# Kernel tuning notes

Hardware: AMD Instinct MI355X
Metric: run time of the kernel (lower is better)

Reference implementation:

```python
import jax, jax.numpy as jnp
import numpy as np

B, S, DM = 2, 2048, 2048
H, KVH, HD = 16, 4, 128
REP = H // KVH  # kv_repeat_factor = 4
ROPE_BASE = 10000.0
EPS = 1e-6


def setup_inputs() -> dict:
    key = jax.random.key(0)
    k0, k1, k2, k3, k4 = jax.random.split(key, 5)
    w = lambda k, o, i: jax.random.normal(k, (o, i), jnp.float32) * (1.0 / np.sqrt(i))
    return {
        "x": jax.random.normal(k0, (B, S, DM), jnp.float32),
        "Wq": w(k1, H * HD, DM),
        "Wk": w(k2, KVH * HD, DM),
        "Wv": w(k3, KVH * HD, DM),
        "Wo": w(k4, DM, H * HD),
    }


def _rope_tables(seq_len, dim):
    inv_freq = 1.0 / (ROPE_BASE ** (jnp.arange(0, dim, 2, dtype=jnp.float32) / dim))
    t = jnp.arange(seq_len, dtype=jnp.float32)
    freqs = jnp.outer(t, inv_freq)            # [S, dim/2]
    emb = jnp.concatenate([freqs, freqs], -1)  # [S, dim]
    return jnp.cos(emb), jnp.sin(emb)


def _rotate_half(x):
    d = x.shape[-1] // 2
    return jnp.concatenate([-x[..., d:], x[..., :d]], axis=-1)


def reference(x, Wq, Wk, Wv, Wo):
    bsz, seq_len, _ = x.shape
    # projections (torch Linear: y = x @ W.T)
    q = (x @ Wq.T).reshape(bsz, seq_len, H, HD).transpose(0, 2, 1, 3)    # [B,H,S,D]
    k = (x @ Wk.T).reshape(bsz, seq_len, KVH, HD).transpose(0, 2, 1, 3)  # [B,KVH,S,D]
    v = (x @ Wv.T).reshape(bsz, seq_len, KVH, HD).transpose(0, 2, 1, 3)
    # rotary embeddings
    cos, sin = _rope_tables(seq_len, HD)  # [S,D]
    cos, sin = cos[None, None], sin[None, None]
    q = q * cos + _rotate_half(q) * sin
    k = k * cos + _rotate_half(k) * sin
    # GQA repeat (repeat_interleave on head dim)
    k = jnp.repeat(k, REP, axis=1)  # [B,H,S,D]
    v = jnp.repeat(v, REP, axis=1)
    # feature map
    qf = jax.nn.elu(q) + 1.0
    kf = jax.nn.elu(k) + 1.0
    # causal linear attention: recurrent kv-state scan over time
    qf_t = qf.transpose(2, 0, 1, 3)  # [S,B,H,D]
    kf_t = kf.transpose(2, 0, 1, 3)
    v_t = v.transpose(2, 0, 1, 3)

    def step(carry, inp):
        state, z = carry                       # [B,H,D,D], [B,H,D]
        q_s, k_s, v_s = inp                    # each [B,H,D]
        state = state + k_s[..., :, None] * v_s[..., None, :]
        z = z + k_s
        num = jnp.einsum('bhe,bhed->bhd', q_s, state)
        den = jnp.einsum('bhe,bhe->bh', q_s, z)[..., None] + EPS
        return (state, z), num / den

    init = (jnp.zeros((bsz, H, HD, HD), x.dtype), jnp.zeros((bsz, H, HD), x.dtype))
    _, out = jax.lax.scan(step, init, (qf_t, kf_t, v_t))  # [S,B,H,D]
    out = out.transpose(1, 0, 2, 3).reshape(bsz, seq_len, H * HD)
    return out @ Wo.T
```

## Files before the change

### kernel.cpp

```cpp
#include <hip/hip_runtime.h>
#include <math.h>
#include <stdint.h>

#define B_ 2
#define S_ 2048
#define H_ 16
#define KVH_ 4
#define HD_ 128
#define NC_ 16
#define CHK_ 128
#define EPS_ 1e-6f
#define GK_ 2048
#define NT_ (GK_ / 32)

typedef __attribute__((ext_vector_type(8))) short short8;
typedef __attribute__((ext_vector_type(4))) float f32x4;

#define GLOAD16(gsrc, sdst) \
    __builtin_amdgcn_global_load_lds((const __attribute__((address_space(1))) unsigned int*)(gsrc), \
                                     (__attribute__((address_space(3))) unsigned int*)(sdst), 16, 0, 0)

static __device__ __forceinline__ float bf2f(unsigned int u) {
    return __uint_as_float(u << 16);
}

static __device__ __forceinline__ void pack8(const float* v, uint4& hi, uint4& lo) {
    unsigned int h[4], l[4];
#pragma unroll
    for (int w = 0; w < 4; w++) {
        unsigned int b0 = __float_as_uint(v[2 * w]);
        unsigned int b1 = __float_as_uint(v[2 * w + 1]);
        unsigned int h0 = b0 & 0xFFFF0000u, h1 = b1 & 0xFFFF0000u;
        h[w] = (h0 >> 16) | h1;
        float r0 = v[2 * w] - __uint_as_float(h0);
        float r1 = v[2 * w + 1] - __uint_as_float(h1);
        l[w] = (__float_as_uint(r0) >> 16) | (__float_as_uint(r1) & 0xFFFF0000u);
    }
    hi = make_uint4(h[0], h[1], h[2], h[3]);
    lo = make_uint4(l[0], l[1], l[2], l[3]);
}

static __device__ __forceinline__ void split8_frag(const float* p, short8& hi, short8& lo) {
#pragma unroll
    for (int e = 0; e < 8; e++) {
        unsigned int b = __float_as_uint(p[e]);
        unsigned int h = b & 0xFFFF0000u;
        hi[e] = (short)(h >> 16);
        float r = p[e] - __uint_as_float(h);
        lo[e] = (short)(__float_as_uint(r) >> 16);
    }
}

__global__ __launch_bounds__(256) void rope_tables_k(float* __restrict__ cost,
                                                     float* __restrict__ sint) {
    int idx = blockIdx.x * 256 + threadIdx.x;
    int j = idx & 63;
    int s = idx >> 6;
    float inv_freq = powf(10000.0f, -(float)(2 * j) / 128.0f);
    float f = (float)s * inv_freq;
    cost[idx] = cosf(f);
    sint[idx] = sinf(f);
}

__global__ __launch_bounds__(256) void split_in_k(
    const float* __restrict__ x,  const float* __restrict__ wq,
    const float* __restrict__ wk, const float* __restrict__ wv,
    unsigned int* __restrict__ xpk,  unsigned int* __restrict__ wqpk,
    unsigned int* __restrict__ wkpk, unsigned int* __restrict__ wvpk)
{
    int g = blockIdx.x * 256 + threadIdx.x;
    const float* in;
    unsigned int* outp;
    int lg;
    if (g < 1048576)      { in = x;  outp = xpk;  lg = g; }
    else if (g < 1572864) { in = wq; outp = wqpk; lg = g - 1048576; }
    else if (g < 1703936) { in = wk; outp = wkpk; lg = g - 1572864; }
    else                  { in = wv; outp = wvpk; lg = g - 1703936; }
    const float* p = in + (size_t)lg * 8;
    float v[8];
    *(float4*)&v[0] = *(const float4*)p;
    *(float4*)&v[4] = *(const float4*)(p + 4);
    uint4 hi, lo;
    pack8(v, hi, lo);
    unsigned int* op = outp + (size_t)lg * 8;
    *(uint4*)op       = hi;
    *(uint4*)(op + 4) = lo;
}

__global__ __launch_bounds__(256) void split_k(const float* __restrict__ in,
                                               unsigned int* __restrict__ outp, int ngrp)
{
    int g = blockIdx.x * 256 + threadIdx.x;
    if (g >= ngrp) return;
    const float* p = in + (size_t)g * 8;
    float x[8];
    *(float4*)&x[0] = *(const float4*)p;
    *(float4*)&x[4] = *(const float4*)(p + 4);
    uint4 hi, lo;
    pack8(x, hi, lo);
    unsigned int* op = outp + (size_t)g * 8;
    *(uint4*)op       = hi;
    *(uint4*)(op + 4) = lo;
}

template <int EPI>
__global__ __launch_bounds__(256, 2) void gemm3_k(
    const char* __restrict__ Apk, const char* __restrict__ W0,
    const char* __restrict__ W1, const char* __restrict__ W2,
    float* __restrict__ Y, int ldY, int nend0, int nend1, int nbx,
    const float* __restrict__ cosT, const float* __restrict__ sinT,
    char* __restrict__ qfo, char* __restrict__ kfo, float* __restrict__ vvo)
{
    __shared__ __attribute__((aligned(16))) char smem[65536];

    int nwg = gridDim.x;
    int bid = blockIdx.x;
    int swz = (bid & 7) * (nwg >> 3) + (bid >> 3);
    int by = swz / nbx, bx = swz % nbx;
    const int m0 = by * 128, n0 = bx * 128;

    const char* Wsel;
    int nw;
    if (n0 < nend0)      { Wsel = W0; nw = n0; }
    else if (n0 < nend1) { Wsel = W1; nw = n0 - nend0; }
    else                 { Wsel = W2; nw = n0 - nend1; }

    const int tid = threadIdx.x;
    const int lane = tid & 63;
    const int wv = tid >> 6;
    const int wr = wv >> 1, wc = wv & 1;

    const int r8 = lane >> 3, sl = lane & 7;
    const char* ap[4];
    const char* wp[4];
    int adst[4], wdst[4];
#pragma unroll
    for (int i = 0; i < 4; i++) {
        int rowA = wv * 32 + i * 8 + r8;
        ap[i] = Apk + (size_t)(m0 + rowA) * (GK_ * 4) + (size_t)((sl ^ (rowA & 7)) * 16);
        wp[i] = Wsel + (size_t)(nw + rowA) * (GK_ * 4) + (size_t)((sl ^ (rowA & 7)) * 16);
        adst[i] = wv * 4096 + i * 1024;
        wdst[i] = 16384 + wv * 4096 + i * 1024;
    }

    const int lrow = lane & 15, lg = lane >> 4, lc7 = lane & 7;
    const int aoff = (wr * 64 + lrow) * 128 + ((((lg << 1)) ^ lc7) << 4);
    const int woff = 16384 + (wc * 64 + lrow) * 128 + ((((lg << 1)) ^ lc7) << 4);

    f32x4 acc[4][4];
#pragma unroll
    for (int i = 0; i < 4; i++)
#pragma unroll
        for (int j = 0; j < 4; j++) acc[i][j] = (f32x4)(0.f);

#pragma unroll
    for (int i = 0; i < 4; i++) {
        GLOAD16(ap[i], smem + adst[i]);
        GLOAD16(wp[i], smem + wdst[i]);
    }
    __syncthreads();

    for (int kt = 0; kt < NT_; ++kt) {
        const int cur = kt & 1;
        if (kt + 1 < NT_) {
            const size_t koff = (size_t)(kt + 1) * 128;
            const int nb = (cur ^ 1) * 32768;
#pragma unroll
            for (int i = 0; i < 4; i++) {
                GLOAD16(ap[i] + koff, smem + nb + adst[i]);
                GLOAD16(wp[i] + koff, smem + nb + wdst[i]);
            }
        }
        const char* sb = smem + cur * 32768;
        short8 ah[4], al[4], bh[4], bl[4];
#pragma unroll
        for (int f = 0; f < 4; f++) {
            ah[f] = *(const short8*)(sb + (aoff)        + f * 2048);
            al[f] = *(const short8*)(sb + (aoff ^ 16)   + f * 2048);
            bh[f] = *(const short8*)(sb + (woff)        + f * 2048);
            bl[f] = *(const short8*)(sb + (woff ^ 16)   + f * 2048);
        }
#pragma unroll
        for (int i = 0; i < 4; i++)
#pragma unroll
            for (int j = 0; j < 4; j++) {
                acc[i][j] = __builtin_amdgcn_mfma_f32_16x16x32_bf16(ah[i], bh[j], acc[i][j], 0, 0, 0);
                acc[i][j] = __builtin_amdgcn_mfma_f32_16x16x32_bf16(ah[i], bl[j], acc[i][j], 0, 0, 0);
                acc[i][j] = __builtin_amdgcn_mfma_f32_16x16x32_bf16(al[i], bh[j], acc[i][j], 0, 0, 0);
            }
        __syncthreads();
    }

    if (EPI == 0) {
#pragma unroll
        for (int i = 0; i < 4; i++) {
            int r0 = m0 + wr * 64 + i * 16 + lg * 4;
#pragma unroll
            for (int j = 0; j < 4; j++) {
                int cc = n0 + wc * 64 + j * 16 + lrow;
                f32x4 v = acc[i][j];
                Y[(size_t)(r0 + 0) * ldY + cc] = v[0];
                Y[(size_t)(r0 + 1) * ldY + cc] = v[1];
                Y[(size_t)(r0 + 2) * ldY + cc] = v[2];
                Y[(size_t)(r0 + 3) * ldY + cc] = v[3];
            }
        }
    } else {
        float* Ct = (float*)smem;
#pragma unroll
        for (int i = 0; i < 4; i++) {
            int r = wr * 64 + i * 16 + lg * 4;
#pragma unroll
            for (int j = 0; j < 4; j++) {
                int ccol = wc * 64 + j * 16 + lrow;
#pragma unroll
                for (int rr = 0; rr < 4; rr++)
                    Ct[(r + rr) * 128 + ccol] = acc[i][j][rr];
            }
        }
        __syncthreads();
        if (n0 < 2560) {
            const int isq = (n0 < 2048) ? 1 : 0;
            const int hh = isq ? (n0 >> 7) : ((n0 - 2048) >> 7);
            char* basep = isq ? qfo : kfo;
            const int bstride = (isq ? H_ : KVH_) * S_;
#pragma unroll
            for (int it = 0; it < 8; it++) {
                int idx = it * 256 + tid;
                int row = idx >> 4, g = idx & 15;
                int midx = m0 + row, bb = midx >> 11, ss = midx & 2047;
                int j0 = g * 8;
                int lowh = (j0 < 64) ? 1 : 0;
                int f0 = lowh ? j0 : j0 - 64;
                float o[8];
#pragma unroll
                for (int e = 0; e < 8; e++) {
                    float cs = cosT[ss * 64 + f0 + e];
                    float sn = sinT[ss * 64 + f0 + e];
                    float a = Ct[row * 128 + j0 + e];
                    float p = Ct[row * 128 + (lowh ? j0 + e + 64 : j0 + e - 64)];
                    float v = lowh ? (a * cs - p * sn) : (a * cs + p * sn);
                    o[e] = v > 0.f ? v + 1.f : expf(v);
                }
                uint4 hi, lo;
                pack8(o, hi, lo);
                char* dst = basep + ((size_t)bb * bstride + (size_t)hh * S_ + ss) * 512 + g * 32;
                *(uint4*)dst        = hi;
                *(uint4*)(dst + 16) = lo;
            }
        } else {
            const int kvh = (n0 - 2560) >> 7;
#pragma unroll
            for (int it = 0; it < 16; it++) {
                int idx = it * 256 + tid;
                int r = idx >> 5, c4 = idx & 31;
                int midx = m0 + r, bb = midx >> 11, ss = midx & 2047;
                *(float4*)(vvo + ((size_t)(bb * KVH_ + kvh) * S_ + ss) * HD_ + c4 * 4) =
                    *(const float4*)(Ct + r * 128 + c4 * 4);
            }
        }
    }
}

__global__ __launch_bounds__(256) void vt_k(const float* __restrict__ vv,
                                            char* __restrict__ vtpk)
{
    __shared__ __attribute__((aligned(16))) float Vt[CHK_][HD_ + 4];
    int bx = blockIdx.x;
    int st = bx & 15;
    int bkv = bx >> 4;
    int tid = threadIdx.x;
#pragma unroll
    for (int it = 0; it < 16; it++) {
        int idx = it * 256 + tid;
        int r = idx >> 5, c4 = idx & 31;
        *(float4*)&Vt[r][c4 * 4] =
            *(const float4*)(vv + ((size_t)bkv * S_ + st * CHK_ + r) * HD_ + c4 * 4);
    }
    __syncthreads();
#pragma unroll
    for (int it = 0; it < 2; it++) {
        int t2 = it * 256 + tid;
        int d = t2 & 127, sg = t2 >> 7;
#pragma unroll
        for (int kk = 0; kk < 4; kk++) {
            int kgl = sg * 4 + kk;
            float f[8];
#pragma unroll
            for (int e = 0; e < 8; e++) f[e] = Vt[kgl * 8 + e][d];
            uint4 hi, lo;
            pack8(f, hi, lo);
            char* op = vtpk + (size_t)bkv * 1048576 + (size_t)d * 8192 + (size_t)(st * 16 + kgl) * 32;
            *(uint4*)op        = hi;
            *(uint4*)(op + 16) = lo;
        }
    }
}

__global__ __launch_bounds__(256) void chunk_kv_k(
    const char* __restrict__ kfpk, const float* __restrict__ vv,
    float* __restrict__ kvc, float* __restrict__ zc)
{
    int bx = blockIdx.x;
    int c = bx % NC_;
    int bkv = bx / NC_;
    const char* kp = kfpk + ((size_t)bkv * S_ + c * CHK_) * 512;
    const float* vp = vv + ((size_t)bkv * S_ + c * CHK_) * HD_;
    __shared__ __attribute__((aligned(16))) float ks[CHK_][HD_ + 4];
    __shared__ __attribute__((aligned(16))) float vs[CHK_][HD_ + 4];
    int tid = threadIdx.x, tx = tid & 15, ty = tid >> 4;
#pragma unroll
    for (int it = 0; it < 8; it++) {
        int idx = it * 256 + tid;
        int r = idx >> 4, kg = idx & 15;
        const uint4* sp = (const uint4*)(kp + (size_t)r * 512 + kg * 32);
        uint4 hi = sp[0], lo = sp[1];
        float* d = &ks[r][kg * 8];
        d[0] = bf2f(hi.x & 0xFFFFu) + bf2f(lo.x & 0xFFFFu);
        d[1] = bf2f(hi.x >> 16)     + bf2f(lo.x >> 16);
        d[2] = bf2f(hi.y & 0xFFFFu) + bf2f(lo.y & 0xFFFFu);
        d[3] = bf2f(hi.y >> 16)     + bf2f(lo.y >> 16);
        d[4] = bf2f(hi.z & 0xFFFFu) + bf2f(lo.z & 0xFFFFu);
        d[5] = bf2f(hi.z >> 16)     + bf2f(lo.z >> 16);
        d[6] = bf2f(hi.w & 0xFFFFu) + bf2f(lo.w & 0xFFFFu);
        d[7] = bf2f(hi.w >> 16)     + bf2f(lo.w >> 16);
    }
#pragma unroll
    for (int it = 0; it < 16; it++) {
        int idx = it * 256 + tid;
        int r = idx >> 5, c4 = idx & 31;
        *(float4*)&vs[r][c4 * 4] = *(const float4*)(vp + (size_t)r * HD_ + c4 * 4);
    }
    __syncthreads();
    float acc[8][8];
#pragma unroll
    for (int i = 0; i < 8; i++)
#pragma unroll
        for (int j = 0; j < 8; j++) acc[i][j] = 0.f;
    for (int j = 0; j < CHK_; j++) {
        float a[8], b[8];
        *(float4*)&a[0] = *(const float4*)&ks[j][ty * 8];
        *(float4*)&a[4] = *(const float4*)&ks[j][ty * 8 + 4];
        *(float4*)&b[0] = *(const float4*)&vs[j][tx * 8];
        *(float4*)&b[4] = *(const float4*)&vs[j][tx * 8 + 4];
#pragma unroll
        for (int i = 0; i < 8; i++)
#pragma unroll
            for (int jj = 0; jj < 8; jj++)
                acc[i][jj] = fmaf(a[i], b[jj], acc[i][jj]);
    }
    float* outp = kvc + (size_t)bx * (HD_ * HD_);
#pragma unroll
    for (int i = 0; i < 8; i++) {
        float* op = outp + (size_t)(ty * 8 + i) * HD_ + tx * 8;
        *(float4*)op       = make_float4(acc[i][0], acc[i][1], acc[i][2], acc[i][3]);
        *(float4*)(op + 4) = make_float4(acc[i][4], acc[i][5], acc[i][6], acc[i][7]);
    }
    if (tid < CHK_) {
        float z = 0.f;
        for (int j = 0; j < CHK_; j++) z += ks[j][tid];
        zc[(size_t)bx * HD_ + tid] = z;
    }
}

__global__ __launch_bounds__(256) void chunk_scan_k(const float* __restrict__ kvc,
                                                    char* __restrict__ kvct,
                                                    float* __restrict__ zc)
{
    int bx = blockIdx.x;
    int bkv = bx >> 3, dg = bx & 7;
    int tid = threadIdx.x;
    int d = dg * 16 + (tid & 15);
    int g8 = tid >> 4;
    float acc[8];
#pragma unroll
    for (int i = 0; i < 8; i++) acc[i] = 0.f;
    float zacc = 0.f;
    for (int c = 0; c < NC_; c++) {
        size_t cb = (size_t)(bkv * NC_ + c);
        const float* p = kvc + cb * 16384;
        float cur[8];
#pragma unroll
        for (int i = 0; i < 8; i++) cur[i] = p[(g8 * 8 + i) * 128 + d];
        uint4 hi, lo;
        pack8(acc, hi, lo);
        char* op = kvct + cb * 65536 + (size_t)d * 512 + g8 * 32;
        *(uint4*)op        = hi;
        *(uint4*)(op + 16) = lo;
#pragma unroll
        for (int i = 0; i < 8; i++) acc[i] += cur[i];
        if (tid < 16) {
            float* zp = zc + cb * 128 + dg * 16 + tid;
            float zcur = *zp;
            *zp = zacc;
            zacc += zcur;
        }
    }
}

__global__ __launch_bounds__(256, 1) void chunk_out_k(
    const char* __restrict__ qfpk, const char* __restrict__ kfpk,
    const char* __restrict__ vtpk, const char* __restrict__ kvct,
    const float* __restrict__ zc, char* __restrict__ attnpk)
{
    __shared__ __attribute__((aligned(16))) char smem[100864];
    char*  stA  = smem;
    char*  stB  = smem + 16384;
    float* Pf   = (float*)(smem + 32768);
    float* zs   = (float*)(smem + 98304);
    float* rsum = (float*)(smem + 98816);
    float* den2 = (float*)(smem + 99840);
    float* den  = (float*)(smem + 100352);

    int bx = blockIdx.x;
    int c = bx & 15, h = (bx >> 4) & 15, b = bx >> 8;
    int kv = h >> 2;
    int bkv = b * KVH_ + kv;
    int bkvc = bkv * NC_ + c;
    const char* Qb  = qfpk + ((size_t)(b * H_ + h) * S_ + c * CHK_) * 512;
    const char* Kb  = kfpk + ((size_t)bkv * S_ + c * CHK_) * 512;
    const char* Vtb = vtpk + (size_t)bkv * 1048576 + (size_t)c * 512;
    const char* Spb = kvct + (size_t)bkvc * 65536;
    const float* zp = zc + (size_t)bkvc * 128;

    int tid = threadIdx.x;
    int lane = tid & 63, wv = tid >> 6;
    int wr = wv >> 1, wc = wv & 1;
    int lrow = lane & 15, lg = lane >> 4, l7 = lane & 7;

    if (tid < 32) *(float4*)(zs + tid * 4) = *(const float4*)(zp + tid * 4);

    const char *qsrc[4], *ksrc[4], *vsrc[4], *ssrc[4];
    char *adst[4], *bdst[4];
#pragma unroll
    for (int i = 0; i < 4; i++) {
        int row = wv * 32 + i * 8 + (lane >> 3);
        int sl = (lane & 7) ^ (row & 7);
        qsrc[i] = Qb  + (size_t)row * 512  + sl * 16;
        ksrc[i] = Kb  + (size_t)row * 512  + sl * 16;
        vsrc[i] = Vtb + (size_t)row * 8192 + sl * 16;
        ssrc[i] = Spb + (size_t)row * 512  + sl * 16;
        adst[i] = stA + wv * 4096 + i * 1024;
        bdst[i] = stB + wv * 4096 + i * 1024;
    }
    int aoffs[4], boffs[4];
#pragma unroll
    for (int f = 0; f < 4; f++) {
        aoffs[f] = (wr * 64 + f * 16 + lrow) * 128 + (((lg << 1) ^ l7) << 4);
        boffs[f] = (wc * 64 + f * 16 + lrow) * 128 + (((lg << 1) ^ l7) << 4);
    }

    f32x4 acc1[4][4];
#pragma unroll
    for (int i = 0; i < 4; i++)
#pragma unroll
        for (int j = 0; j < 4; j++) acc1[i][j] = (f32x4)(0.f);

    for (int s = 0; s < 4; s++) {
#pragma unroll
        for (int i = 0; i < 4; i++) {
            GLOAD16(qsrc[i] + s * 128, adst[i]);
            GLOAD16(ksrc[i] + s * 128, bdst[i]);
        }
        __syncthreads();
        short8 ah[4], al[4], bh[4], bl[4];
#pragma unroll
        for (int f = 0; f < 4; f++) {
            ah[f] = *(const short8*)(stA + aoffs[f]);
            al[f] = *(const short8*)(stA + (aoffs[f] ^ 16));
            bh[f] = *(const short8*)(stB + boffs[f]);
            bl[f] = *(const short8*)(stB + (boffs[f] ^ 16));
        }
#pragma unroll
        for (int i = 0; i < 4; i++)
#pragma unroll
            for (int j = 0; j < 4; j++) {
                acc1[i][j] = __builtin_amdgcn_mfma_f32_16x16x32_bf16(ah[i], bh[j], acc1[i][j], 0, 0, 0);
                acc1[i][j] = __builtin_amdgcn_mfma_f32_16x16x32_bf16(ah[i], bl[j], acc1[i][j], 0, 0, 0);
                acc1[i][j] = __builtin_amdgcn_mfma_f32_16x16x32_bf16(al[i], bh[j], acc1[i][j], 0, 0, 0);
            }
        __syncthreads();
    }

#pragma unroll
    for (int fi = 0; fi < 4; fi++) {
#pragma unroll
        for (int reg = 0; reg < 4; reg++) {
            int i = wr * 64 + fi * 16 + lg * 4 + reg;
            float rsv = 0.f;
#pragma unroll
            for (int fj = 0; fj < 4; fj++) {
                int j = wc * 64 + fj * 16 + lrow;
                float v = (j <= i) ? acc1[fi][fj][reg] : 0.f;
                rsv += v;
                Pf[i * 128 + (((j >> 3) ^ (i & 7)) << 3) + (j & 7)] = v;
            }
#pragma unroll
            for (int m = 1; m < 16; m <<= 1) rsv += __shfl_xor(rsv, m, 64);
            if (lrow == 0) rsum[i * 2 + wc] = rsv;
        }
    }

    f32x4 acc2[4][4];
#pragma unroll
    for (int i = 0; i < 4; i++)
#pragma unroll
        for (int j = 0; j < 4; j++) acc2[i][j] = (f32x4)(0.f);
    float d2a[4] = {0.f, 0.f, 0.f, 0.f};

    for (int s = 0; s < 4; s++) {
#pragma unroll
        for (int i = 0; i < 4; i++) {
            GLOAD16(qsrc[i] + s * 128, adst[i]);
            GLOAD16(ssrc[i] + s * 128, bdst[i]);
        }
        __syncthreads();
        short8 ah[4], al[4], bh[4], bl[4];
#pragma unroll
        for (int f = 0; f < 4; f++) {
            ah[f] = *(const short8*)(stA + aoffs[f]);
            al[f] = *(const short8*)(stA + (aoffs[f] ^ 16));
            bh[f] = *(const short8*)(stB + boffs[f]);
            bl[f] = *(const short8*)(stB + (boffs[f] ^ 16));
        }
        float zv[8];
#pragma unroll
        for (int e = 0; e < 8; e++) zv[e] = zs[s * 32 + lg * 8 + e];
#pragma unroll
        for (int f = 0; f < 4; f++)
#pragma unroll
            for (int e = 0; e < 8; e++)
                d2a[f] += (bf2f((unsigned int)(unsigned short)ah[f][e]) +
                           bf2f((unsigned int)(unsigned short)al[f][e])) * zv[e];
#pragma unroll
        for (int i = 0; i < 4; i++)
#pragma unroll
            for (int j = 0; j < 4; j++) {
                acc2[i][j] = __builtin_amdgcn_mfma_f32_16x16x32_bf16(ah[i], bh[j], acc2[i][j], 0, 0, 0);
                acc2[i][j] = __builtin_amdgcn_mfma_f32_16x16x32_bf16(ah[i], bl[j], acc2[i][j], 0, 0, 0);
                acc2[i][j] = __builtin_amdgcn_mfma_f32_16x16x32_bf16(al[i], bh[j], acc2[i][j], 0, 0, 0);
            }
        __syncthreads();
    }
#pragma unroll
    for (int f = 0; f < 4; f++) {
        float v = d2a[f];
        v += __shfl_xor(v, 16, 64);
        v += __shfl_xor(v, 32, 64);
        if (wc == 0 && lg == 0) den2[wr * 64 + f * 16 + lrow] = v;
    }

    for (int s = 0; s < 4; s++) {
#pragma unroll
        for (int i = 0; i < 4; i++) GLOAD16(vsrc[i] + s * 128, bdst[i]);
        __syncthreads();
        short8 ph[4], pl[4], bh[4], bl[4];
#pragma unroll
        for (int f = 0; f < 4; f++) {
            int i = wr * 64 + f * 16 + lrow;
            int g = (s * 4 + lg) ^ (i & 7);
            float pv[8];
            *(float4*)&pv[0] = *(const float4*)(Pf + i * 128 + g * 8);
            *(float4*)&pv[4] = *(const float4*)(Pf + i * 128 + g * 8 + 4);
            split8_frag(pv, ph[f], pl[f]);
            bh[f] = *(const short8*)(stB + boffs[f]);
            bl[f] = *(const short8*)(stB + (boffs[f] ^ 16));
        }
#pragma unroll
        for (int i = 0; i < 4; i++)
#pragma unroll
            for (int j = 0; j < 4; j++) {
                acc2[i][j] = __builtin_amdgcn_mfma_f32_16x16x32_bf16(ph[i], bh[j], acc2[i][j], 0, 0, 0);
                acc2[i][j] = __builtin_amdgcn_mfma_f32_16x16x32_bf16(ph[i], bl[j], acc2[i][j], 0, 0, 0);
                acc2[i][j] = __builtin_amdgcn_mfma_f32_16x16x32_bf16(pl[i], bh[j], acc2[i][j], 0, 0, 0);
            }
        __syncthreads();
    }

    if (tid < 128) den[tid] = rsum[tid * 2] + rsum[tid * 2 + 1] + den2[tid] + EPS_;
    __syncthreads();
#pragma unroll
    for (int fi = 0; fi < 4; fi++) {
#pragma unroll
        for (int reg = 0; reg < 4; reg++) {
            int i = wr * 64 + fi * 16 + lg * 4 + reg;
            float inv = 1.0f / den[i];
#pragma unroll
            for (int fd = 0; fd < 4; fd++) {
                int d = wc * 64 + fd * 16 + lrow;
                Pf[i * 128 + (((d >> 3) ^ (i & 7)) << 3) + (d & 7)] = acc2[fi][fd][reg] * inv;
            }
        }
    }
    __syncthreads();
    int s0 = c * CHK_;
#pragma unroll
    for (int it = 0; it < 8; it++) {
        int idx = it * 256 + tid;
        int row = idx >> 4, kg = idx & 15;
        int g = kg ^ (row & 7);
        float f[8];
        *(float4*)&f[0] = *(const float4*)(Pf + row * 128 + g * 8);
        *(float4*)&f[4] = *(const float4*)(Pf + row * 128 + g * 8 + 4);
        uint4 hi, lo;
        pack8(f, hi, lo);
        char* op = attnpk + ((size_t)(b * S_ + s0 + row) * 256 + h * 16 + kg) * 32;
        *(uint4*)op        = hi;
        *(uint4*)(op + 16) = lo;
    }
}

extern "C" void kernel_launch(void* const* d_in, const int* in_sizes, int n_in,
                              void* d_out, int out_size, void* d_ws, size_t ws_size,
                              hipStream_t stream)
{
    (void)in_sizes; (void)n_in; (void)out_size; (void)ws_size;
    const float* x  = (const float*)d_in[0];
    const float* Wq = (const float*)d_in[1];
    const float* Wk = (const float*)d_in[2];
    const float* Wv = (const float*)d_in[3];
    const float* Wo = (const float*)d_in[4];
    float* out = (float*)d_out;
    float* ws  = (float*)d_ws;

    float* xpk   = ws;
    float* wqpk  = ws + 8388608;
    float* wkpk  = ws + 12582912;
    float* wvpk  = ws + 13631488;
    char*  qfpk  = (char*)(ws + 14680064);
    char*  kfpk  = (char*)(ws + 23068672);
    float* vv    = ws + 25165824;
    float* cost  = ws + 27262976;
    float* sint  = ws + 27394048;
    float* zc    = ws + 27525120;
    char*  vtpk   = (char*)(ws + 8388608);
    float* kvc    = ws + 10485760;
    char*  kvct   = (char*)(ws + 12582912);
    char*  attnpk = (char*)ws;
    float* wopk   = ws + 8388608;

    rope_tables_k<<<512, 256, 0, stream>>>(cost, sint);

    split_in_k<<<7168, 256, 0, stream>>>(x, Wq, Wk, Wv,
                                         (unsigned int*)xpk, (unsigned int*)wqpk,
                                         (unsigned int*)wkpk, (unsigned int*)wvpk);
    gemm3_k<1><<<768, 256, 0, stream>>>((const char*)xpk, (const char*)wqpk,
                                        (const char*)wkpk, (const char*)wvpk,
                                        nullptr, 0, 2048, 2560, 24,
                                        cost, sint, qfpk, kfpk, vv);

    vt_k<<<128, 256, 0, stream>>>(vv, vtpk);

    chunk_kv_k<<<B_ * KVH_ * NC_, 256, 0, stream>>>(kfpk, vv, kvc, zc);
    chunk_scan_k<<<64, 256, 0, stream>>>(kvc, kvct, zc);
    chunk_out_k<<<B_ * H_ * NC_, 256, 0, stream>>>(qfpk, kfpk, vtpk, kvct, zc, attnpk);

    split_k<<<2048, 256, 0, stream>>>(Wo, (unsigned int*)wopk, 524288);
    gemm3_k<0><<<512, 256, 0, stream>>>((const char*)attnpk, (const char*)wopk,
                                        (const char*)wopk, (const char*)wopk,
                                        out, 2048, 1 << 30, 1 << 30, 16,
                                        nullptr, nullptr, nullptr, nullptr, nullptr);
}
```

Before: 426.6 us.

## Rework projection GEMMs to 8-wave 256x128 tiles with triple-buffered LDS pipeline

The split-bf16 GEMM kernel now runs 512 threads (8 waves) per block on a 256x128 output tile, with a 3-stage LDS ring buffer (144 KB) that prefetches two K-steps ahead. Global-to-LDS loads are interleaved between the two MFMA halves, waits use explicit vmcnt counts, and MFMA sections are wrapped in setprio. The aim is to hide global load latency and halve redundant weight traffic per output. In exchange, each CU holds only one block, fewer blocks are launched, and the epilogue's shared-memory reuse and explicit waitcnt bookkeeping are more fragile.

```diff
diff --git a/kernel.cpp b/kernel.cpp
--- a/kernel.cpp
+++ b/kernel.cpp
@@ -11,7 +11,7 @@
 #define CHK_ 128
 #define EPS_ 1e-6f
 #define GK_ 2048
-#define NT_ (GK_ / 32)
+#define NT8_ (GK_ / 32)
 
 typedef __attribute__((ext_vector_type(8))) short short8;
 typedef __attribute__((ext_vector_type(4))) float f32x4;
@@ -19,6 +19,8 @@
 #define GLOAD16(gsrc, sdst) \
     __builtin_amdgcn_global_load_lds((const __attribute__((address_space(1))) unsigned int*)(gsrc), \
                                      (__attribute__((address_space(3))) unsigned int*)(sdst), 16, 0, 0)
+
+#define MFMA_B16(a, b, c) __builtin_amdgcn_mfma_f32_16x16x32_bf16((a), (b), (c), 0, 0, 0)
 
 static __device__ __forceinline__ float bf2f(unsigned int u) {
     return __uint_as_float(u << 16);
@@ -104,20 +106,20 @@
 }
 
 template <int EPI>
-__global__ __launch_bounds__(256, 2) void gemm3_k(
+__global__ __launch_bounds__(512, 1) void gemm8_k(
     const char* __restrict__ Apk, const char* __restrict__ W0,
     const char* __restrict__ W1, const char* __restrict__ W2,
     float* __restrict__ Y, int ldY, int nend0, int nend1, int nbx,
     const float* __restrict__ cosT, const float* __restrict__ sinT,
     char* __restrict__ qfo, char* __restrict__ kfo, float* __restrict__ vvo)
 {
-    __shared__ __attribute__((aligned(16))) char smem[65536];
+    __shared__ __attribute__((aligned(16))) char smem[147456];
 
     int nwg = gridDim.x;
     int bid = blockIdx.x;
     int swz = (bid & 7) * (nwg >> 3) + (bid >> 3);
     int by = swz / nbx, bx = swz % nbx;
-    const int m0 = by * 128, n0 = bx * 128;
+    const int m0 = by * 256, n0 = bx * 128;
 
     const char* Wsel;
     int nw;
@@ -128,24 +130,32 @@
     const int tid = threadIdx.x;
     const int lane = tid & 63;
     const int wv = tid >> 6;
-    const int wr = wv >> 1, wc = wv & 1;
+    const int wm = wv >> 1, wn = wv & 1;
 
     const int r8 = lane >> 3, sl = lane & 7;
-    const char* ap[4];
-    const char* wp[4];
-    int adst[4], wdst[4];
+    const char* asrc[4];
+    const char* bsrc[2];
+    int adst[4], bdst[2];
 #pragma unroll
     for (int i = 0; i < 4; i++) {
         int rowA = wv * 32 + i * 8 + r8;
-        ap[i] = Apk + (size_t)(m0 + rowA) * (GK_ * 4) + (size_t)((sl ^ (rowA & 7)) * 16);
-        wp[i] = Wsel + (size_t)(nw + rowA) * (GK_ * 4) + (size_t)((sl ^ (rowA & 7)) * 16);
+        asrc[i] = Apk + (size_t)(m0 + rowA) * (GK_ * 4) + (size_t)((sl ^ (rowA & 7)) * 16);
         adst[i] = wv * 4096 + i * 1024;
-        wdst[i] = 16384 + wv * 4096 + i * 1024;
+    }
+#pragma unroll
+    for (int j = 0; j < 2; j++) {
+        int rowB = wv * 16 + j * 8 + r8;
+        bsrc[j] = Wsel + (size_t)(nw + rowB) * (GK_ * 4) + (size_t)((sl ^ (rowB & 7)) * 16);
+        bdst[j] = 32768 + wv * 2048 + j * 1024;
     }
 
     const int lrow = lane & 15, lg = lane >> 4, lc7 = lane & 7;
-    const int aoff = (wr * 64 + lrow) * 128 + ((((lg << 1)) ^ lc7) << 4);
-    const int woff = 16384 + (wc * 64 + lrow) * 128 + ((((lg << 1)) ^ lc7) << 4);
+    int aoff[4], boff[4];
+#pragma unroll
+    for (int f = 0; f < 4; f++) {
+        aoff[f] = (wm * 64 + f * 16 + lrow) * 128 + (((lg << 1) ^ lc7) << 4);
+        boff[f] = 32768 + (wn * 64 + f * 16 + lrow) * 128 + (((lg << 1) ^ lc7) << 4);
+    }
 
     f32x4 acc[4][4];
 #pragma unroll
@@ -154,50 +164,88 @@
         for (int j = 0; j < 4; j++) acc[i][j] = (f32x4)(0.f);
 
 #pragma unroll
-    for (int i = 0; i < 4; i++) {
-        GLOAD16(ap[i], smem + adst[i]);
-        GLOAD16(wp[i], smem + wdst[i]);
-    }
-    __syncthreads();
-
-    for (int kt = 0; kt < NT_; ++kt) {
-        const int cur = kt & 1;
-        if (kt + 1 < NT_) {
-            const size_t koff = (size_t)(kt + 1) * 128;
-            const int nb = (cur ^ 1) * 32768;
-#pragma unroll
-            for (int i = 0; i < 4; i++) {
-                GLOAD16(ap[i] + koff, smem + nb + adst[i]);
-                GLOAD16(wp[i] + koff, smem + nb + wdst[i]);
-            }
-        }
-        const char* sb = smem + cur * 32768;
-        short8 ah[4], al[4], bh[4], bl[4];
+    for (int i = 0; i < 4; i++) GLOAD16(asrc[i], smem + adst[i]);
+#pragma unroll
+    for (int j = 0; j < 2; j++) GLOAD16(bsrc[j], smem + bdst[j]);
+#pragma unroll
+    for (int i = 0; i < 4; i++) GLOAD16(asrc[i] + 128, smem + 49152 + adst[i]);
+#pragma unroll
+    for (int j = 0; j < 2; j++) GLOAD16(bsrc[j] + 128, smem + 49152 + bdst[j]);
+    asm volatile("s_waitcnt vmcnt(6)" ::: "memory");
+    __builtin_amdgcn_s_barrier();
+    __builtin_amdgcn_sched_barrier(0);
+
+#pragma unroll 1
+    for (int kt = 0; kt < NT8_; ++kt) {
+        const char* sb = smem + (kt % 3) * 49152;
+        char* stp = smem + ((kt + 2) % 3) * 49152;
+        const size_t koff = (size_t)(kt + 2) * 128;
+        const bool st = (kt + 2 < NT8_);
+
+        if (st) {
+            GLOAD16(asrc[0] + koff, stp + adst[0]);
+            GLOAD16(asrc[1] + koff, stp + adst[1]);
+            GLOAD16(asrc[2] + koff, stp + adst[2]);
+        }
+        short8 bh[4], bl[4];
 #pragma unroll
         for (int f = 0; f < 4; f++) {
-            ah[f] = *(const short8*)(sb + (aoff)        + f * 2048);
-            al[f] = *(const short8*)(sb + (aoff ^ 16)   + f * 2048);
-            bh[f] = *(const short8*)(sb + (woff)        + f * 2048);
-            bl[f] = *(const short8*)(sb + (woff ^ 16)   + f * 2048);
-        }
-#pragma unroll
-        for (int i = 0; i < 4; i++)
+            bh[f] = *(const short8*)(sb + boff[f]);
+            bl[f] = *(const short8*)(sb + (boff[f] ^ 16));
+        }
+        short8 a0h = *(const short8*)(sb + aoff[0]);
+        short8 a0l = *(const short8*)(sb + (aoff[0] ^ 16));
+        short8 a1h = *(const short8*)(sb + aoff[1]);
+        short8 a1l = *(const short8*)(sb + (aoff[1] ^ 16));
+        __builtin_amdgcn_s_setprio(1);
+#pragma unroll
+        for (int j = 0; j < 4; j++) {
+            acc[0][j] = MFMA_B16(a0h, bh[j], acc[0][j]);
+            acc[0][j] = MFMA_B16(a0h, bl[j], acc[0][j]);
+            acc[0][j] = MFMA_B16(a0l, bh[j], acc[0][j]);
+            acc[1][j] = MFMA_B16(a1h, bh[j], acc[1][j]);
+            acc[1][j] = MFMA_B16(a1h, bl[j], acc[1][j]);
+            acc[1][j] = MFMA_B16(a1l, bh[j], acc[1][j]);
+        }
+        __builtin_amdgcn_s_setprio(0);
+        __builtin_amdgcn_s_barrier();
+
+        if (st) {
+            GLOAD16(asrc[3] + koff, stp + adst[3]);
+            GLOAD16(bsrc[0] + koff, stp + bdst[0]);
+            GLOAD16(bsrc[1] + koff, stp + bdst[1]);
+        }
+        short8 a2h = *(const short8*)(sb + aoff[2]);
+        short8 a2l = *(const short8*)(sb + (aoff[2] ^ 16));
+        short8 a3h = *(const short8*)(sb + aoff[3]);
+        short8 a3l = *(const short8*)(sb + (aoff[3] ^ 16));
+        __builtin_amdgcn_s_setprio(1);
+#pragma unroll
+        for (int j = 0; j < 4; j++) {
+            acc[2][j] = MFMA_B16(a2h, bh[j], acc[2][j]);
+            acc[2][j] = MFMA_B16(a2h, bl[j], acc[2][j]);
+            acc[2][j] = MFMA_B16(a2l, bh[j], acc[2][j]);
+            acc[3][j] = MFMA_B16(a3h, bh[j], acc[3][j]);
+            acc[3][j] = MFMA_B16(a3h, bl[j], acc[3][j]);
+            acc[3][j] = MFMA_B16(a3l, bh[j], acc[3][j]);
+        }
+        __builtin_amdgcn_s_setprio(0);
+        if (kt < NT8_ - 2) {
+            asm volatile("s_waitcnt vmcnt(6)" ::: "memory");
+        } else if (kt == NT8_ - 2) {
+            asm volatile("s_waitcnt vmcnt(0)" ::: "memory");
+        }
+        __builtin_amdgcn_s_barrier();
+        __builtin_amdgcn_sched_barrier(0);
+    }
+
+    if (EPI == 0) {
+#pragma unroll
+        for (int i = 0; i < 4; i++) {
+            int r0 = m0 + wm * 64 + i * 16 + lg * 4;
 #pragma unroll
             for (int j = 0; j < 4; j++) {
-                acc[i][j] = __builtin_amdgcn_mfma_f32_16x16x32_bf16(ah[i], bh[j], acc[i][j], 0, 0, 0);
-                acc[i][j] = __builtin_amdgcn_mfma_f32_16x16x32_bf16(ah[i], bl[j], acc[i][j], 0, 0, 0);
-                acc[i][j] = __builtin_amdgcn_mfma_f32_16x16x32_bf16(al[i], bh[j], acc[i][j], 0, 0, 0);
-            }
-        __syncthreads();
-    }
-
-    if (EPI == 0) {
-#pragma unroll
-        for (int i = 0; i < 4; i++) {
-            int r0 = m0 + wr * 64 + i * 16 + lg * 4;
-#pragma unroll
-            for (int j = 0; j < 4; j++) {
-                int cc = n0 + wc * 64 + j * 16 + lrow;
+                int cc = n0 + wn * 64 + j * 16 + lrow;
                 f32x4 v = acc[i][j];
                 Y[(size_t)(r0 + 0) * ldY + cc] = v[0];
                 Y[(size_t)(r0 + 1) * ldY + cc] = v[1];
@@ -209,10 +257,10 @@
         float* Ct = (float*)smem;
 #pragma unroll
         for (int i = 0; i < 4; i++) {
-            int r = wr * 64 + i * 16 + lg * 4;
+            int r = wm * 64 + i * 16 + lg * 4;
 #pragma unroll
             for (int j = 0; j < 4; j++) {
-                int ccol = wc * 64 + j * 16 + lrow;
+                int ccol = wn * 64 + j * 16 + lrow;
 #pragma unroll
                 for (int rr = 0; rr < 4; rr++)
                     Ct[(r + rr) * 128 + ccol] = acc[i][j][rr];
@@ -226,7 +274,7 @@
             const int bstride = (isq ? H_ : KVH_) * S_;
 #pragma unroll
             for (int it = 0; it < 8; it++) {
-                int idx = it * 256 + tid;
+                int idx = it * 512 + tid;
                 int row = idx >> 4, g = idx & 15;
                 int midx = m0 + row, bb = midx >> 11, ss = midx & 2047;
                 int j0 = g * 8;
@@ -252,7 +300,7 @@
             const int kvh = (n0 - 2560) >> 7;
 #pragma unroll
             for (int it = 0; it < 16; it++) {
-                int idx = it * 256 + tid;
+                int idx = it * 512 + tid;
                 int r = idx >> 5, c4 = idx & 31;
                 int midx = m0 + r, bb = midx >> 11, ss = midx & 2047;
                 *(float4*)(vvo + ((size_t)(bb * KVH_ + kvh) * S_ + ss) * HD_ + c4 * 4) =
@@ -475,9 +523,9 @@
         for (int i = 0; i < 4; i++)
 #pragma unroll
             for (int j = 0; j < 4; j++) {
-                acc1[i][j] = __builtin_amdgcn_mfma_f32_16x16x32_bf16(ah[i], bh[j], acc1[i][j], 0, 0, 0);
-                acc1[i][j] = __builtin_amdgcn_mfma_f32_16x16x32_bf16(ah[i], bl[j], acc1[i][j], 0, 0, 0);
-                acc1[i][j] = __builtin_amdgcn_mfma_f32_16x16x32_bf16(al[i], bh[j], acc1[i][j], 0, 0, 0);
+                acc1[i][j] = MFMA_B16(ah[i], bh[j], acc1[i][j]);
+                acc1[i][j] = MFMA_B16(ah[i], bl[j], acc1[i][j]);
+                acc1[i][j] = MFMA_B16(al[i], bh[j], acc1[i][j]);
             }
         __syncthreads();
     }
@@ -536,9 +584,9 @@
         for (int i = 0; i < 4; i++)
 #pragma unroll
             for (int j = 0; j < 4; j++) {
-                acc2[i][j] = __builtin_amdgcn_mfma_f32_16x16x32_bf16(ah[i], bh[j], acc2[i][j], 0, 0, 0);
-                acc2[i][j] = __builtin_amdgcn_mfma_f32_16x16x32_bf16(ah[i], bl[j], acc2[i][j], 0, 0, 0);
-                acc2[i][j] = __builtin_amdgcn_mfma_f32_16x16x32_bf16(al[i], bh[j], acc2[i][j], 0, 0, 0);
+                acc2[i][j] = MFMA_B16(ah[i], bh[j], acc2[i][j]);
+                acc2[i][j] = MFMA_B16(ah[i], bl[j], acc2[i][j]);
+                acc2[i][j] = MFMA_B16(al[i], bh[j], acc2[i][j]);
             }
         __syncthreads();
     }
@@ -570,9 +618,9 @@
         for (int i = 0; i < 4; i++)
 #pragma unroll
             for (int j = 0; j < 4; j++) {
-                acc2[i][j] = __builtin_amdgcn_mfma_f32_16x16x32_bf16(ph[i], bh[j], acc2[i][j], 0, 0, 0);
-                acc2[i][j] = __builtin_amdgcn_mfma_f32_16x16x32_bf16(ph[i], bl[j], acc2[i][j], 0, 0, 0);
-                acc2[i][j] = __builtin_amdgcn_mfma_f32_16x16x32_bf16(pl[i], bh[j], acc2[i][j], 0, 0, 0);
+                acc2[i][j] = MFMA_B16(ph[i], bh[j], acc2[i][j]);
+                acc2[i][j] = MFMA_B16(ph[i], bl[j], acc2[i][j]);
+                acc2[i][j] = MFMA_B16(pl[i], bh[j], acc2[i][j]);
             }
         __syncthreads();
     }
@@ -644,7 +692,7 @@
     split_in_k<<<7168, 256, 0, stream>>>(x, Wq, Wk, Wv,
                                          (unsigned int*)xpk, (unsigned int*)wqpk,
                                          (unsigned int*)wkpk, (unsigned int*)wvpk);
-    gemm3_k<1><<<768, 256, 0, stream>>>((const char*)xpk, (const char*)wqpk,
+    gemm8_k<1><<<384, 512, 0, stream>>>((const char*)xpk, (const char*)wqpk,
                                         (const char*)wkpk, (const char*)wvpk,
                                         nullptr, 0, 2048, 2560, 24,
                                         cost, sint, qfpk, kfpk, vv);
@@ -656,7 +704,7 @@
     chunk_out_k<<<B_ * H_ * NC_, 256, 0, stream>>>(qfpk, kfpk, vtpk, kvct, zc, attnpk);
 
     split_k<<<2048, 256, 0, stream>>>(Wo, (unsigned int*)wopk, 524288);
-    gemm3_k<0><<<512, 256, 0, stream>>>((const char*)attnpk, (const char*)wopk,
+    gemm8_k<0><<<256, 512, 0, stream>>>((const char*)attnpk, (const char*)wopk,
                                         (const char*)wopk, (const char*)wopk,
                                         out, 2048, 1 << 30, 1 << 30, 16,
                                         nullptr, nullptr, nullptr, nullptr, nullptr);
```

New measurement: 468.9 us. 1.1x slower.

## Fuse rope tables into split kernel and V transpose into chunk KV kernel

Applied to the files above, without the earlier changes.

Folds the rope cos/sin table generation into the input split kernel as extra blocks, and merges the V-transpose/pack kernel into the per-chunk KV state kernel. The chunk KV kernel is also split along the key dimension into two halves, which doubles the block count from 128 to 256 and halves per-thread accumulators. This removes two kernel launches and a separate reload of V, and improves occupancy of a small-grid kernel. The trade-off is that the half-1 blocks carry extra transpose work, which creates some load imbalance, and each block still loads the full V chunk.

```diff
diff --git a/kernel.cpp b/kernel.cpp
--- a/kernel.cpp
+++ b/kernel.cpp
@@ -20,6 +20,8 @@
     __builtin_amdgcn_global_load_lds((const __attribute__((address_space(1))) unsigned int*)(gsrc), \
                                      (__attribute__((address_space(3))) unsigned int*)(sdst), 16, 0, 0)
 
+#define MFMA_B16(a, b, c) __builtin_amdgcn_mfma_f32_16x16x32_bf16((a), (b), (c), 0, 0, 0)
+
 static __device__ __forceinline__ float bf2f(unsigned int u) {
     return __uint_as_float(u << 16);
 }
@@ -51,24 +53,24 @@
     }
 }
 
-__global__ __launch_bounds__(256) void rope_tables_k(float* __restrict__ cost,
-                                                     float* __restrict__ sint) {
-    int idx = blockIdx.x * 256 + threadIdx.x;
-    int j = idx & 63;
-    int s = idx >> 6;
-    float inv_freq = powf(10000.0f, -(float)(2 * j) / 128.0f);
-    float f = (float)s * inv_freq;
-    cost[idx] = cosf(f);
-    sint[idx] = sinf(f);
-}
-
 __global__ __launch_bounds__(256) void split_in_k(
     const float* __restrict__ x,  const float* __restrict__ wq,
     const float* __restrict__ wk, const float* __restrict__ wv,
     unsigned int* __restrict__ xpk,  unsigned int* __restrict__ wqpk,
-    unsigned int* __restrict__ wkpk, unsigned int* __restrict__ wvpk)
+    unsigned int* __restrict__ wkpk, unsigned int* __restrict__ wvpk,
+    float* __restrict__ cost, float* __restrict__ sint)
 {
     int g = blockIdx.x * 256 + threadIdx.x;
+    if (g >= 1835008) {
+        int idx = g - 1835008;
+        int j = idx & 63;
+        int s = idx >> 6;
+        float inv_freq = powf(10000.0f, -(float)(2 * j) / 128.0f);
+        float f = (float)s * inv_freq;
+        cost[idx] = cosf(f);
+        sint[idx] = sinf(f);
+        return;
+    }
     const float* in;
     unsigned int* outp;
     int lg;
@@ -184,9 +186,9 @@
         for (int i = 0; i < 4; i++)
 #pragma unroll
             for (int j = 0; j < 4; j++) {
-                acc[i][j] = __builtin_amdgcn_mfma_f32_16x16x32_bf16(ah[i], bh[j], acc[i][j], 0, 0, 0);
-                acc[i][j] = __builtin_amdgcn_mfma_f32_16x16x32_bf16(ah[i], bl[j], acc[i][j], 0, 0, 0);
-                acc[i][j] = __builtin_amdgcn_mfma_f32_16x16x32_bf16(al[i], bh[j], acc[i][j], 0, 0, 0);
+                acc[i][j] = MFMA_B16(ah[i], bh[j], acc[i][j]);
+                acc[i][j] = MFMA_B16(ah[i], bl[j], acc[i][j]);
+                acc[i][j] = MFMA_B16(al[i], bh[j], acc[i][j]);
             }
         __syncthreads();
     }
@@ -262,60 +264,26 @@
     }
 }
 
-__global__ __launch_bounds__(256) void vt_k(const float* __restrict__ vv,
-                                            char* __restrict__ vtpk)
-{
-    __shared__ __attribute__((aligned(16))) float Vt[CHK_][HD_ + 4];
-    int bx = blockIdx.x;
-    int st = bx & 15;
-    int bkv = bx >> 4;
-    int tid = threadIdx.x;
-#pragma unroll
-    for (int it = 0; it < 16; it++) {
-        int idx = it * 256 + tid;
-        int r = idx >> 5, c4 = idx & 31;
-        *(float4*)&Vt[r][c4 * 4] =
-            *(const float4*)(vv + ((size_t)bkv * S_ + st * CHK_ + r) * HD_ + c4 * 4);
-    }
-    __syncthreads();
-#pragma unroll
-    for (int it = 0; it < 2; it++) {
-        int t2 = it * 256 + tid;
-        int d = t2 & 127, sg = t2 >> 7;
-#pragma unroll
-        for (int kk = 0; kk < 4; kk++) {
-            int kgl = sg * 4 + kk;
-            float f[8];
-#pragma unroll
-            for (int e = 0; e < 8; e++) f[e] = Vt[kgl * 8 + e][d];
-            uint4 hi, lo;
-            pack8(f, hi, lo);
-            char* op = vtpk + (size_t)bkv * 1048576 + (size_t)d * 8192 + (size_t)(st * 16 + kgl) * 32;
-            *(uint4*)op        = hi;
-            *(uint4*)(op + 16) = lo;
-        }
-    }
-}
-
-__global__ __launch_bounds__(256) void chunk_kv_k(
+__global__ __launch_bounds__(256) void chunk_kvt_k(
     const char* __restrict__ kfpk, const float* __restrict__ vv,
-    float* __restrict__ kvc, float* __restrict__ zc)
+    float* __restrict__ kvc, float* __restrict__ zc, char* __restrict__ vtpk)
 {
     int bx = blockIdx.x;
-    int c = bx % NC_;
-    int bkv = bx / NC_;
+    int eh = bx & 1;
+    int c = (bx >> 1) & 15;
+    int bkv = bx >> 5;
     const char* kp = kfpk + ((size_t)bkv * S_ + c * CHK_) * 512;
     const float* vp = vv + ((size_t)bkv * S_ + c * CHK_) * HD_;
-    __shared__ __attribute__((aligned(16))) float ks[CHK_][HD_ + 4];
+    __shared__ __attribute__((aligned(16))) float ks[CHK_][68];
     __shared__ __attribute__((aligned(16))) float vs[CHK_][HD_ + 4];
     int tid = threadIdx.x, tx = tid & 15, ty = tid >> 4;
 #pragma unroll
-    for (int it = 0; it < 8; it++) {
+    for (int it = 0; it < 4; it++) {
         int idx = it * 256 + tid;
-        int r = idx >> 4, kg = idx & 15;
-        const uint4* sp = (const uint4*)(kp + (size_t)r * 512 + kg * 32);
+        int r = idx >> 3, kg8 = idx & 7;
+        const uint4* sp = (const uint4*)(kp + (size_t)r * 512 + (eh * 8 + kg8) * 32);
         uint4 hi = sp[0], lo = sp[1];
-        float* d = &ks[r][kg * 8];
+        float* d = &ks[r][kg8 * 8];
         d[0] = bf2f(hi.x & 0xFFFFu) + bf2f(lo.x & 0xFFFFu);
         d[1] = bf2f(hi.x >> 16)     + bf2f(lo.x >> 16);
         d[2] = bf2f(hi.y & 0xFFFFu) + bf2f(lo.y & 0xFFFFu);
@@ -332,34 +300,52 @@
         *(float4*)&vs[r][c4 * 4] = *(const float4*)(vp + (size_t)r * HD_ + c4 * 4);
     }
     __syncthreads();
-    float acc[8][8];
-#pragma unroll
-    for (int i = 0; i < 8; i++)
+    float acc[4][8];
+#pragma unroll
+    for (int i = 0; i < 4; i++)
 #pragma unroll
         for (int j = 0; j < 8; j++) acc[i][j] = 0.f;
     for (int j = 0; j < CHK_; j++) {
-        float a[8], b[8];
-        *(float4*)&a[0] = *(const float4*)&ks[j][ty * 8];
-        *(float4*)&a[4] = *(const float4*)&ks[j][ty * 8 + 4];
+        float a[4], b[8];
+        *(float4*)&a[0] = *(const float4*)&ks[j][ty * 4];
         *(float4*)&b[0] = *(const float4*)&vs[j][tx * 8];
         *(float4*)&b[4] = *(const float4*)&vs[j][tx * 8 + 4];
 #pragma unroll
-        for (int i = 0; i < 8; i++)
+        for (int i = 0; i < 4; i++)
 #pragma unroll
             for (int jj = 0; jj < 8; jj++)
                 acc[i][jj] = fmaf(a[i], b[jj], acc[i][jj]);
     }
-    float* outp = kvc + (size_t)bx * (HD_ * HD_);
-#pragma unroll
-    for (int i = 0; i < 8; i++) {
-        float* op = outp + (size_t)(ty * 8 + i) * HD_ + tx * 8;
+    float* outp = kvc + (size_t)(bkv * NC_ + c) * (HD_ * HD_);
+#pragma unroll
+    for (int i = 0; i < 4; i++) {
+        float* op = outp + (size_t)(eh * 64 + ty * 4 + i) * HD_ + tx * 8;
         *(float4*)op       = make_float4(acc[i][0], acc[i][1], acc[i][2], acc[i][3]);
         *(float4*)(op + 4) = make_float4(acc[i][4], acc[i][5], acc[i][6], acc[i][7]);
     }
-    if (tid < CHK_) {
+    if (tid < 64) {
         float z = 0.f;
         for (int j = 0; j < CHK_; j++) z += ks[j][tid];
-        zc[(size_t)bx * HD_ + tid] = z;
+        zc[(size_t)(bkv * NC_ + c) * HD_ + eh * 64 + tid] = z;
+    }
+    if (eh == 1) {
+#pragma unroll
+        for (int it = 0; it < 2; it++) {
+            int t2 = it * 256 + tid;
+            int d = t2 & 127, sg = t2 >> 7;
+#pragma unroll
+            for (int kk = 0; kk < 4; kk++) {
+                int kgl = sg * 4 + kk;
+                float f[8];
+#pragma unroll
+                for (int e = 0; e < 8; e++) f[e] = vs[kgl * 8 + e][d];
+                uint4 hi, lo;
+                pack8(f, hi, lo);
+                char* op = vtpk + (size_t)bkv * 1048576 + (size_t)d * 8192 + (size_t)(c * 16 + kgl) * 32;
+                *(uint4*)op        = hi;
+                *(uint4*)(op + 16) = lo;
+            }
+        }
     }
 }
 
@@ -475,9 +461,9 @@
         for (int i = 0; i < 4; i++)
 #pragma unroll
             for (int j = 0; j < 4; j++) {
-                acc1[i][j] = __builtin_amdgcn_mfma_f32_16x16x32_bf16(ah[i], bh[j], acc1[i][j], 0, 0, 0);
-                acc1[i][j] = __builtin_amdgcn_mfma_f32_16x16x32_bf16(ah[i], bl[j], acc1[i][j], 0, 0, 0);
-                acc1[i][j] = __builtin_amdgcn_mfma_f32_16x16x32_bf16(al[i], bh[j], acc1[i][j], 0, 0, 0);
+                acc1[i][j] = MFMA_B16(ah[i], bh[j], acc1[i][j]);
+                acc1[i][j] = MFMA_B16(ah[i], bl[j], acc1[i][j]);
+                acc1[i][j] = MFMA_B16(al[i], bh[j], acc1[i][j]);
             }
         __syncthreads();
     }
@@ -536,9 +522,9 @@
         for (int i = 0; i < 4; i++)
 #pragma unroll
             for (int j = 0; j < 4; j++) {
-                acc2[i][j] = __builtin_amdgcn_mfma_f32_16x16x32_bf16(ah[i], bh[j], acc2[i][j], 0, 0, 0);
-                acc2[i][j] = __builtin_amdgcn_mfma_f32_16x16x32_bf16(ah[i], bl[j], acc2[i][j], 0, 0, 0);
-                acc2[i][j] = __builtin_amdgcn_mfma_f32_16x16x32_bf16(al[i], bh[j], acc2[i][j], 0, 0, 0);
+                acc2[i][j] = MFMA_B16(ah[i], bh[j], acc2[i][j]);
+                acc2[i][j] = MFMA_B16(ah[i], bl[j], acc2[i][j]);
+                acc2[i][j] = MFMA_B16(al[i], bh[j], acc2[i][j]);
             }
         __syncthreads();
     }
@@ -570,9 +556,9 @@
         for (int i = 0; i < 4; i++)
 #pragma unroll
             for (int j = 0; j < 4; j++) {
-                acc2[i][j] = __builtin_amdgcn_mfma_f32_16x16x32_bf16(ph[i], bh[j], acc2[i][j], 0, 0, 0);
-                acc2[i][j] = __builtin_amdgcn_mfma_f32_16x16x32_bf16(ph[i], bl[j], acc2[i][j], 0, 0, 0);
-                acc2[i][j] = __builtin_amdgcn_mfma_f32_16x16x32_bf16(pl[i], bh[j], acc2[i][j], 0, 0, 0);
+                acc2[i][j] = MFMA_B16(ph[i], bh[j], acc2[i][j]);
+                acc2[i][j] = MFMA_B16(ph[i], bl[j], acc2[i][j]);
+                acc2[i][j] = MFMA_B16(pl[i], bh[j], acc2[i][j]);
             }
         __syncthreads();
     }
@@ -639,19 +625,16 @@
     char*  attnpk = (char*)ws;
     float* wopk   = ws + 8388608;
 
-    rope_tables_k<<<512, 256, 0, stream>>>(cost, sint);
-
-    split_in_k<<<7168, 256, 0, stream>>>(x, Wq, Wk, Wv,
+    split_in_k<<<7680, 256, 0, stream>>>(x, Wq, Wk, Wv,
                                          (unsigned int*)xpk, (unsigned int*)wqpk,
-                                         (unsigned int*)wkpk, (unsigned int*)wvpk);
+                                         (unsigned int*)wkpk, (unsigned int*)wvpk,
+                                         cost, sint);
     gemm3_k<1><<<768, 256, 0, stream>>>((const char*)xpk, (const char*)wqpk,
                                         (const char*)wkpk, (const char*)wvpk,
                                         nullptr, 0, 2048, 2560, 24,
                                         cost, sint, qfpk, kfpk, vv);
 
-    vt_k<<<128, 256, 0, stream>>>(vv, vtpk);
-
-    chunk_kv_k<<<B_ * KVH_ * NC_, 256, 0, stream>>>(kfpk, vv, kvc, zc);
+    chunk_kvt_k<<<256, 256, 0, stream>>>(kfpk, vv, kvc, zc, vtpk);
     chunk_scan_k<<<64, 256, 0, stream>>>(kvc, kvct, zc);
     chunk_out_k<<<B_ * H_ * NC_, 256, 0, stream>>>(qfpk, kfpk, vtpk, kvct, zc, attnpk);
 
```

Result: faster. 418.0 us (-2.0%).
